# Performance work log

Measured on AMD Instinct MI355X. Metric: run time of the kernel, lower is better.

The kernel has to match this reference:

```python
import jax, jax.numpy as jnp
import numpy as np

B, CIN, H, W = 16, 20, 256, 256
WIDTH, M1, M2, NLAYERS, FC_HID, COUT = 64, 16, 16, 4, 128, 20


def setup_inputs() -> dict:
    key = jax.random.key(0)
    ks = jax.random.split(key, 16)
    scale = 1.0 / (WIDTH * WIDTH)  # matches torch: scale * rand(..., cfloat)
    u = lambda k, s: scale * jax.random.uniform(k, s, dtype=jnp.float32)
    n = lambda k, s: 0.05 * jax.random.normal(k, s, dtype=jnp.float32)
    return {
        "x": jax.random.normal(ks[0], (B, CIN, H, W), dtype=jnp.float32),
        # complex spectral weights stored as real/imag pairs, stacked over 4 layers
        "spec_w1r": u(ks[1], (NLAYERS, WIDTH, WIDTH, M1, M2)),
        "spec_w1i": u(ks[2], (NLAYERS, WIDTH, WIDTH, M1, M2)),
        "spec_w2r": u(ks[3], (NLAYERS, WIDTH, WIDTH, M1, M2)),
        "spec_w2i": u(ks[4], (NLAYERS, WIDTH, WIDTH, M1, M2)),
        # 1x1 conv weights (out, in) and biases, stacked over 4 layers
        "pw_w": n(ks[5], (NLAYERS, WIDTH, WIDTH)),
        "pw_b": n(ks[6], (NLAYERS, WIDTH)),
        "fc0_w": n(ks[7], (WIDTH, CIN)),
        "fc0_b": n(ks[8], (WIDTH,)),
        "fc1_w": n(ks[9], (FC_HID, WIDTH)),
        "fc1_b": n(ks[10], (FC_HID,)),
        "fc2_w": n(ks[11], (COUT, FC_HID)),
        "fc2_b": n(ks[12], (COUT,)),
    }


def _spectral_conv(h, w1, w2):
    # h: (B, WIDTH, H, W) real; w1,w2: (WIDTH, WIDTH, M1, M2) complex
    b, c, hh, ww = h.shape
    x_ft = jnp.fft.rfft2(h)  # (B, WIDTH, H, W//2+1) complex64
    top = jnp.einsum('bixy,ioxy->boxy', x_ft[:, :, :M1, :M2], w1)
    bot = jnp.einsum('bixy,ioxy->boxy', x_ft[:, :, -M1:, :M2], w2)
    out_ft = jnp.zeros((b, c, hh, ww // 2 + 1), dtype=jnp.complex64)
    out_ft = out_ft.at[:, :, :M1, :M2].set(top).at[:, :, -M1:, :M2].set(bot)
    return jnp.fft.irfft2(out_ft, s=(hh, ww))


def reference(x, spec_w1r, spec_w1i, spec_w2r, spec_w2i, pw_w, pw_b,
              fc0_w, fc0_b, fc1_w, fc1_b, fc2_w, fc2_b):
    gelu = lambda t: jax.nn.gelu(t, approximate=False)  # torch F.gelu default = erf
    # lift: permute to channels-last, Linear(20->width), back to channels-first
    h = jnp.einsum('bchw,dc->bdhw', x, fc0_w) + fc0_b[None, :, None, None]
    for i in range(NLAYERS):
        w1 = spec_w1r[i] + 1j * spec_w1i[i]
        w2 = spec_w2r[i] + 1j * spec_w2i[i]
        x1 = _spectral_conv(h, w1, w2)
        x2 = jnp.einsum('bihw,oi->bohw', h, pw_w[i]) + pw_b[i][None, :, None, None]
        h = x1 + x2
        if i < NLAYERS - 1:  # no GELU after the 4th block in the original
            h = gelu(h)
    h = jnp.einsum('bchw,dc->bdhw', h, fc1_w) + fc1_b[None, :, None, None]
    h = gelu(h)
    h = jnp.einsum('bchw,dc->bdhw', h, fc2_w) + fc2_b[None, :, None, None]
    return h  # (B, 20, H, W)
```

## Files before the change

kernel.cpp:

```cpp
#include <hip/hip_runtime.h>
#include <hip/hip_bf16.h>


#define HW_TOT 65536
#define PI2_256 0.024543692606170259758f

__device__ __forceinline__ float gelu_exact(float v) {
    return 0.5f * v * (1.0f + erff(v * 0.70710678118654752440f));
}
__device__ __forceinline__ float gelu_fast(float v) {
    float z  = v * 0.70710678118654752440f;
    float az = fabsf(z);
    float t  = __builtin_amdgcn_rcpf(fmaf(0.3275911f, az, 1.0f));
    float p  = t * (0.254829592f + t * (-0.284496736f + t * (1.421413741f +
               t * (-1.453152027f + t * 1.061405429f))));
    float e  = __expf(-az * az);
    float er = copysignf(1.0f - p * e, z);
    return 0.5f * v * (1.0f + er);
}
#define F4COMP(v, k) ((k)==0?(v).x:(k)==1?(v).y:(k)==2?(v).z:(v).w)

template<int CI, int CO, int WS>
__global__ void __launch_bounds__(256) conv1x1_kernel(
    const float* __restrict__ in, const float* __restrict__ w,
    const float* __restrict__ bias, float* __restrict__ out)
{
    const int b = blockIdx.y;
    const int p = blockIdx.x * 256 + threadIdx.x;
    const float* inp = in + (size_t)b * CI * HW_TOT + p;
    float acc[CO];
#pragma unroll
    for (int o = 0; o < CO; ++o) acc[o] = bias[o];
    for (int ci = 0; ci < CI; ++ci) {
        float hv = inp[(size_t)ci * HW_TOT];
#pragma unroll
        for (int o = 0; o < CO; ++o)
            acc[o] = fmaf(w[o * WS + ci], hv, acc[o]);
    }
    float* op = out + (size_t)b * CO * HW_TOT + p;
#pragma unroll
    for (int o = 0; o < CO; ++o) op[(size_t)o * HW_TOT] = acc[o];
}

__global__ void __launch_bounds__(256) dfty_kernel(
    const float* __restrict__ h, float* __restrict__ T)
{
    __shared__ float As[128][68];
    __shared__ float Wc[64][32];
    __shared__ float cs2[256], sn2[256];
    const int t = threadIdx.x;
    {
        float a = (float)t * PI2_256;
        cs2[t] = cosf(a); sn2[t] = sinf(a);
    }
    __syncthreads();

    const size_t rowbase = (size_t)blockIdx.x * 128;
    const int jg = t & 7, rg = t >> 3;
    float acc[4][4];
#pragma unroll
    for (int k = 0; k < 4; ++k)
#pragma unroll
        for (int q = 0; q < 4; ++q) acc[k][q] = 0.0f;

    for (int yc = 0; yc < 256; yc += 64) {
        if (yc) __syncthreads();
#pragma unroll
        for (int it = 0; it < 8; ++it) {
            int idx = t + 256 * it;
            int rr = idx >> 4, c4 = idx & 15;
            float4 v = *(const float4*)(h + (rowbase + rr) * 256 + yc + c4 * 4);
            *(float4*)&As[rr][c4 * 4] = v;
        }
#pragma unroll
        for (int it = 0; it < 8; ++it) {
            int i = t + 256 * it;
            int yl = i >> 5, j = i & 31, ky = j >> 1;
            int m = ((yc + yl) * ky) & 255;
            Wc[yl][j] = (j & 1) ? -sn2[m] : cs2[m];
        }
        __syncthreads();
#pragma unroll 2
        for (int yy = 0; yy < 64; yy += 4) {
            float4 wv[4], av[4];
#pragma unroll
            for (int q = 0; q < 4; ++q) wv[q] = *(const float4*)&Wc[yy + q][jg * 4];
#pragma unroll
            for (int k = 0; k < 4; ++k) av[k] = *(const float4*)&As[rg + 32 * k][yy];
#pragma unroll
            for (int k = 0; k < 4; ++k)
#pragma unroll
                for (int q = 0; q < 4; ++q) {
                    float a = F4COMP(av[k], q);
                    acc[k][0] = fmaf(a, wv[q].x, acc[k][0]);
                    acc[k][1] = fmaf(a, wv[q].y, acc[k][1]);
                    acc[k][2] = fmaf(a, wv[q].z, acc[k][2]);
                    acc[k][3] = fmaf(a, wv[q].w, acc[k][3]);
                }
        }
    }
#pragma unroll
    for (int k = 0; k < 4; ++k) {
        float4 v = make_float4(acc[k][0], acc[k][1], acc[k][2], acc[k][3]);
        *(float4*)&T[(rowbase + rg + 32 * k) * 32 + jg * 4] = v;
    }
}

__global__ void __launch_bounds__(512) dft2_kernel(
    const float2* __restrict__ T2, float2* __restrict__ X2)
{
    __shared__ float cs[256], sn[256];
    const int t = threadIdx.x;
    if (t < 256) {
        float a = (float)t * PI2_256;
        cs[t] = cosf(a); sn[t] = sinf(a);
    }
    __syncthreads();
    const int bc = blockIdx.x;
    const int ky = t & 15, kxi = t >> 4;
    const int kx = (kxi < 16) ? kxi : (224 + kxi);
    const float2* Tp = T2 + (size_t)bc * 4096 + ky;
    float xr = 0.0f, xi = 0.0f;
    int m = 0;
    for (int x = 0; x < 256; ++x) {
        float2 tv = Tp[(size_t)x * 16];
        float c = cs[m], s = sn[m];
        xr = fmaf(tv.x, c, fmaf(tv.y, s, xr));
        xi = fmaf(tv.y, c, fmaf(-tv.x, s, xi));
        m = (m + kx) & 255;
    }
    X2[(size_t)bc * 512 + t] = make_float2(xr, xi);
}

__global__ void __launch_bounds__(512) mix_kernel(
    const float2* __restrict__ X2, float2* __restrict__ Y2,
    const float* __restrict__ w1r, const float* __restrict__ w1i,
    const float* __restrict__ w2r, const float* __restrict__ w2i, int layer)
{
    const int bo = blockIdx.x;
    const int b = bo >> 6, o = bo & 63;
    const int t = threadIdx.x;
    const int ky = t & 15, kxi = t >> 4;
    const bool top = (kxi < 16);
    const int kxm = top ? kxi : (kxi - 16);
    const float* wr = top ? w1r : w2r;
    const float* wi = top ? w1i : w2i;
    float yr = 0.0f, yi = 0.0f;
    for (int i = 0; i < 64; ++i) {
        float2 xv = X2[((size_t)(b * 64 + i) * 32 + kxi) * 16 + ky];
        size_t widx = (((size_t)layer * 64 + i) * 64 + o) * 256 + (kxm * 16 + ky);
        float wrv = wr[widx], wiv = wi[widx];
        yr = fmaf(xv.x, wrv, fmaf(-xv.y, wiv, yr));
        yi = fmaf(xv.x, wiv, fmaf(xv.y, wrv, yi));
    }
    Y2[((size_t)(b * 64 + o) * 32 + kxi) * 16 + ky] = make_float2(yr, yi);
}

__global__ void __launch_bounds__(256) idft1_kernel(
    const float2* __restrict__ Y2, float2* __restrict__ G2)
{
    __shared__ float cs[256], sn[256];
    const int t = threadIdx.x;
    {
        float a = (float)t * PI2_256;
        cs[t] = cosf(a); sn[t] = sinf(a);
    }
    __syncthreads();
    const int bo = blockIdx.x >> 4;
    const int xc = blockIdx.x & 15;
    const int ky = t & 15, xo = t >> 4;
    const int x = xc * 16 + xo;
    const float2* Yp = Y2 + (size_t)bo * 512 + ky;
    float gr = 0.0f, gi = 0.0f;
    for (int kxi = 0; kxi < 32; ++kxi) {
        float2 yv = Yp[(size_t)kxi * 16];
        int kx = (kxi < 16) ? kxi : (224 + kxi);
        int m = (kx * x) & 255;
        float c = cs[m], s = sn[m];
        gr = fmaf(yv.x, c, fmaf(-yv.y, s, gr));
        gi = fmaf(yv.x, s, fmaf(yv.y, c, gi));
    }
    G2[((size_t)bo * 256 + x) * 16 + ky] = make_float2(gr, gi);
}

__global__ void __launch_bounds__(1024, 8) pwcomb_kernel(
    float* __restrict__ h, const float2* __restrict__ G2,
    const float* __restrict__ pw_w, const float* __restrict__ pw_b,
    int layer, int do_gelu)
{
    __shared__ float buf[20480];
    float (*hs)[256] = (float (*)[256])buf;
    float (*Wt)[64]  = (float (*)[64])(buf + 16384);
    float (*Gt)[64]  = (float (*)[64])buf;
    float (*Pt)[256] = (float (*)[256])(buf + 2048);
    const int t = threadIdx.x;
    const int b = blockIdx.x >> 8;
    const int x = blockIdx.x & 255;

    const float* wl = pw_w + layer * 4096;
#pragma unroll
    for (int it = 0; it < 4; ++it) {
        int i = t + 1024 * it;
        int o = i & 63, ci = i >> 6;
        Wt[ci][o] = wl[o * 64 + ci];
    }
#pragma unroll
    for (int it = 0; it < 4; ++it) {
        int idx = t + 1024 * it;
        int ci = idx >> 6, c4 = idx & 63;
        float4 v = *(const float4*)(h + ((size_t)(b * 64 + ci) * 256 + x) * 256 + c4 * 4);
        *(float4*)&hs[ci][c4 * 4] = v;
    }
    __syncthreads();

    const int og = t & 15, yg = t >> 4;
    const float* bl = pw_b + layer * 64;
    float acc[4][4];
#pragma unroll
    for (int oj = 0; oj < 4; ++oj) {
        float bv = bl[og * 4 + oj];
#pragma unroll
        for (int yj = 0; yj < 4; ++yj) acc[yj][oj] = bv;
    }
    for (int ci = 0; ci < 64; ++ci) {
        float4 hv = *(const float4*)&hs[ci][yg * 4];
        float4 wv = *(const float4*)&Wt[ci][og * 4];
#pragma unroll
        for (int yj = 0; yj < 4; ++yj) {
            float a = F4COMP(hv, yj);
            acc[yj][0] = fmaf(a, wv.x, acc[yj][0]);
            acc[yj][1] = fmaf(a, wv.y, acc[yj][1]);
            acc[yj][2] = fmaf(a, wv.z, acc[yj][2]);
            acc[yj][3] = fmaf(a, wv.w, acc[yj][3]);
        }
    }
    __syncthreads();

    {
        int o = t >> 4, ky = t & 15;
        float2 g = G2[((size_t)(b * 64 + o) * 256 + x) * 16 + ky];
        Gt[2 * ky][o] = g.x;
        Gt[2 * ky + 1][o] = g.y;
    }
    const float inv = 1.0f / 65536.0f;
#pragma unroll
    for (int it = 0; it < 8; ++it) {
        int i = t + 1024 * it;
        int jp = i >> 8, y = i & 255, ky = jp >> 1;
        int m = (ky * y) & 255;
        float wk = (ky == 0) ? inv : 2.0f * inv;
        float ang = (float)m * PI2_256;
        Pt[jp][y] = (jp & 1) ? -wk * sinf(ang) : wk * cosf(ang);
    }
    __syncthreads();

#pragma unroll 4
    for (int jp = 0; jp < 32; ++jp) {
        float4 pv = *(const float4*)&Pt[jp][yg * 4];
        float4 gv = *(const float4*)&Gt[jp][og * 4];
#pragma unroll
        for (int yj = 0; yj < 4; ++yj) {
            float a = F4COMP(pv, yj);
            acc[yj][0] = fmaf(a, gv.x, acc[yj][0]);
            acc[yj][1] = fmaf(a, gv.y, acc[yj][1]);
            acc[yj][2] = fmaf(a, gv.z, acc[yj][2]);
            acc[yj][3] = fmaf(a, gv.w, acc[yj][3]);
        }
    }
#pragma unroll
    for (int oj = 0; oj < 4; ++oj) {
        float4 v;
        v.x = acc[0][oj]; v.y = acc[1][oj]; v.z = acc[2][oj]; v.w = acc[3][oj];
        if (do_gelu) {
            v.x = gelu_fast(v.x); v.y = gelu_fast(v.y);
            v.z = gelu_fast(v.z); v.w = gelu_fast(v.w);
        }
        *(float4*)&h[((size_t)(b * 64 + og * 4 + oj) * 256 + x) * 256 + yg * 4] = v;
    }
}

__global__ void __launch_bounds__(256) transpose_w1_kernel(
    const float* __restrict__ w1, float* __restrict__ w1t)
{
    int i = blockIdx.x * 256 + threadIdx.x;
    int ci = i >> 7, hd = i & 127;
    w1t[i] = w1[hd * 64 + ci];
}

__global__ void __launch_bounds__(512, 4) proj_kernel(
    const float* __restrict__ h,
    const float* __restrict__ w1t, const float* __restrict__ b1,
    const float* __restrict__ w2, const float* __restrict__ b2,
    float* __restrict__ out)
{
    __shared__ float hs[64][128];
    __shared__ float red[4][20][128];
    const int t = threadIdx.x;
    const int blk = blockIdx.x;
    const int b = blk >> 9;
    const int p0 = (blk & 511) << 7;

    {
        const float* hp = h + (size_t)b * 64 * HW_TOT + p0;
#pragma unroll
        for (int it = 0; it < 4; ++it) {
            int idx = t + 512 * it;
            int ci = idx >> 5, c4 = idx & 31;
            float4 v = *(const float4*)(hp + (size_t)ci * HW_TOT + c4 * 4);
            *(float4*)&hs[ci][c4 * 4] = v;
        }
    }
    __syncthreads();

    const int px = t & 127;
    const int wv = __builtin_amdgcn_readfirstlane(t >> 7);
    const int hd0 = wv * 32;

    float acc[32];
#pragma unroll
    for (int k = 0; k < 32; ++k) acc[k] = b1[hd0 + k];
#pragma unroll 2
    for (int ci = 0; ci < 64; ++ci) {
        float a = hs[ci][px];
        const float* wr = w1t + ci * 128 + hd0;
#pragma unroll
        for (int k = 0; k < 32; ++k) acc[k] = fmaf(wr[k], a, acc[k]);
    }
#pragma unroll
    for (int k = 0; k < 32; ++k) acc[k] = gelu_fast(acc[k]);

    float acc2[20];
#pragma unroll
    for (int o = 0; o < 20; ++o) {
        const float* w2r = w2 + o * 128 + hd0;
        float s0 = (wv == 0) ? b2[o] : 0.0f, s1 = 0.0f;
#pragma unroll
        for (int k = 0; k < 32; k += 2) {
            s0 = fmaf(w2r[k], acc[k], s0);
            s1 = fmaf(w2r[k + 1], acc[k + 1], s1);
        }
        acc2[o] = s0 + s1;
    }
#pragma unroll
    for (int o = 0; o < 20; ++o) red[wv][o][px] = acc2[o];
    __syncthreads();

    const int og = t >> 7;
    float* op = out + (size_t)b * 20 * HW_TOT + p0 + px;
#pragma unroll
    for (int j = 0; j < 5; ++j) {
        int o = og * 5 + j;
        float s = red[0][o][px] + red[1][o][px] + red[2][o][px] + red[3][o][px];
        op[(size_t)o * HW_TOT] = s;
    }
}

extern "C" void kernel_launch(void* const* d_in, const int* in_sizes, int n_in,
                              void* d_out, int out_size, void* d_ws, size_t ws_size,
                              hipStream_t stream)
{
    const float* x     = (const float*)d_in[0];
    const float* w1r   = (const float*)d_in[1];
    const float* w1i   = (const float*)d_in[2];
    const float* w2r   = (const float*)d_in[3];
    const float* w2i   = (const float*)d_in[4];
    const float* pw_w  = (const float*)d_in[5];
    const float* pw_b  = (const float*)d_in[6];
    const float* fc0_w = (const float*)d_in[7];
    const float* fc0_b = (const float*)d_in[8];
    const float* fc1_w = (const float*)d_in[9];
    const float* fc1_b = (const float*)d_in[10];
    const float* fc2_w = (const float*)d_in[11];
    const float* fc2_b = (const float*)d_in[12];
    float* out = (float*)d_out;
    float* ws  = (float*)d_ws;

    const size_t per_sample_floats = 4849664;
    int CB = 16;
    while (CB > 1 && (size_t)CB * per_sample_floats * 4 > ws_size) CB >>= 1;

    float*  h  = ws;
    float*  T  = ws + (size_t)CB * 4194304;
    float2* T2 = (float2*)T;
    float2* X2 = (float2*)(T + (size_t)CB * 524288);
    float2* Y2 = (float2*)(T + (size_t)CB * 524288 + (size_t)CB * 65536);
    float2* G2 = T2;

    for (int c0 = 0; c0 < 16; c0 += CB) {
        const float* xc = x + (size_t)c0 * 20 * HW_TOT;
        float* oc = out + (size_t)c0 * 20 * HW_TOT;

        conv1x1_kernel<20, 64, 20>
            <<<dim3(256, CB), 256, 0, stream>>>(xc, fc0_w, fc0_b, h);

        for (int l = 0; l < 4; ++l) {
            dfty_kernel <<<CB * 128, 256, 0, stream>>>(h, T);
            dft2_kernel <<<CB * 64, 512, 0, stream>>>(T2, X2);
            mix_kernel  <<<CB * 64, 512, 0, stream>>>(X2, Y2, w1r, w1i, w2r, w2i, l);
            idft1_kernel<<<CB * 64 * 16, 256, 0, stream>>>(Y2, G2);
            pwcomb_kernel<<<CB * 256, 1024, 0, stream>>>(h, G2, pw_w, pw_b, l, (l < 3) ? 1 : 0);
        }

        transpose_w1_kernel<<<32, 256, 0, stream>>>(fc1_w, T);
        proj_kernel<<<CB * 512, 512, 0, stream>>>(h, T, fc1_b, fc2_w, fc2_b, oc);
    }
}
```

Baseline: 2.613 ms.

## Fuse final projection MLP into last layer's pointwise-combine kernel

The last FNO layer's pwcomb kernel now keeps its output tile in shared memory and directly applies the fc1+GELU+fc2 projection, writing the final output. This removes the write of h after layer 4 and the separate proj_kernel's reread of it, roughly 256MB of HBM traffic per chunk. The fused kernel runs at 1024 threads, which adds register pressure and extra syncs. The transposed fc1 weights go into the Y2 buffer, which is safe because idft1 has already consumed it.

```diff
diff --git a/kernel.cpp b/kernel.cpp
--- a/kernel.cpp
+++ b/kernel.cpp
@@ -183,10 +183,14 @@
     G2[((size_t)bo * 256 + x) * 16 + ky] = make_float2(gr, gi);
 }
 
+template<int FUSE>
 __global__ void __launch_bounds__(1024, 8) pwcomb_kernel(
     float* __restrict__ h, const float2* __restrict__ G2,
     const float* __restrict__ pw_w, const float* __restrict__ pw_b,
-    int layer, int do_gelu)
+    int layer, int do_gelu,
+    const float* __restrict__ w1t, const float* __restrict__ fb1,
+    const float* __restrict__ fw2, const float* __restrict__ fb2,
+    float* __restrict__ out)
 {
     __shared__ float buf[20480];
     float (*hs)[256] = (float (*)[256])buf;
@@ -267,15 +271,74 @@
             acc[yj][3] = fmaf(a, gv.w, acc[yj][3]);
         }
     }
+
+    if (!FUSE) {
+#pragma unroll
+        for (int oj = 0; oj < 4; ++oj) {
+            float4 v;
+            v.x = acc[0][oj]; v.y = acc[1][oj]; v.z = acc[2][oj]; v.w = acc[3][oj];
+            if (do_gelu) {
+                v.x = gelu_fast(v.x); v.y = gelu_fast(v.y);
+                v.z = gelu_fast(v.z); v.w = gelu_fast(v.w);
+            }
+            *(float4*)&h[((size_t)(b * 64 + og * 4 + oj) * 256 + x) * 256 + yg * 4] = v;
+        }
+        return;
+    }
+
+    __syncthreads();
 #pragma unroll
     for (int oj = 0; oj < 4; ++oj) {
-        float4 v;
-        v.x = acc[0][oj]; v.y = acc[1][oj]; v.z = acc[2][oj]; v.w = acc[3][oj];
-        if (do_gelu) {
-            v.x = gelu_fast(v.x); v.y = gelu_fast(v.y);
-            v.z = gelu_fast(v.z); v.w = gelu_fast(v.w);
-        }
-        *(float4*)&h[((size_t)(b * 64 + og * 4 + oj) * 256 + x) * 256 + yg * 4] = v;
+        float4 v = make_float4(acc[0][oj], acc[1][oj], acc[2][oj], acc[3][oj]);
+        *(float4*)&buf[(og * 4 + oj) * 260 + yg * 4] = v;
+    }
+    __syncthreads();
+
+    const int px = t & 255;
+    const int wf = __builtin_amdgcn_readfirstlane(t >> 8);
+    float acc2[20];
+#pragma unroll
+    for (int o = 0; o < 20; ++o) acc2[o] = (wf == 0) ? fb2[o] : 0.0f;
+
+#pragma unroll
+    for (int pass = 0; pass < 2; ++pass) {
+        const int hd0 = wf * 32 + pass * 16;
+        float fa[16];
+#pragma unroll
+        for (int k = 0; k < 16; ++k) fa[k] = fb1[hd0 + k];
+#pragma unroll 2
+        for (int ci = 0; ci < 64; ++ci) {
+            float a = buf[ci * 260 + px];
+            const float* wr = w1t + ci * 128 + hd0;
+#pragma unroll
+            for (int k = 0; k < 16; ++k) fa[k] = fmaf(wr[k], a, fa[k]);
+        }
+#pragma unroll
+        for (int k = 0; k < 16; ++k) fa[k] = gelu_fast(fa[k]);
+#pragma unroll
+        for (int o = 0; o < 20; ++o) {
+            const float* w2r = fw2 + o * 128 + hd0;
+            float s0 = 0.0f, s1 = 0.0f;
+#pragma unroll
+            for (int k = 0; k < 16; k += 2) {
+                s0 = fmaf(w2r[k], fa[k], s0);
+                s1 = fmaf(w2r[k + 1], fa[k + 1], s1);
+            }
+            acc2[o] += s0 + s1;
+        }
+    }
+    __syncthreads();
+#pragma unroll
+    for (int o = 0; o < 20; ++o) buf[(wf * 20 + o) * 256 + px] = acc2[o];
+    __syncthreads();
+
+    float* op = out + (size_t)b * 20 * HW_TOT + x * 256 + px;
+#pragma unroll
+    for (int j = 0; j < 5; ++j) {
+        int o = wf * 5 + j;
+        float s = buf[o * 256 + px] + buf[(20 + o) * 256 + px]
+                + buf[(40 + o) * 256 + px] + buf[(60 + o) * 256 + px];
+        op[(size_t)o * HW_TOT] = s;
     }
 }
 
@@ -285,74 +348,6 @@
     int i = blockIdx.x * 256 + threadIdx.x;
     int ci = i >> 7, hd = i & 127;
     w1t[i] = w1[hd * 64 + ci];
-}
-
-__global__ void __launch_bounds__(512, 4) proj_kernel(
-    const float* __restrict__ h,
-    const float* __restrict__ w1t, const float* __restrict__ b1,
-    const float* __restrict__ w2, const float* __restrict__ b2,
-    float* __restrict__ out)
-{
-    __shared__ float hs[64][128];
-    __shared__ float red[4][20][128];
-    const int t = threadIdx.x;
-    const int blk = blockIdx.x;
-    const int b = blk >> 9;
-    const int p0 = (blk & 511) << 7;
-
-    {
-        const float* hp = h + (size_t)b * 64 * HW_TOT + p0;
-#pragma unroll
-        for (int it = 0; it < 4; ++it) {
-            int idx = t + 512 * it;
-            int ci = idx >> 5, c4 = idx & 31;
-            float4 v = *(const float4*)(hp + (size_t)ci * HW_TOT + c4 * 4);
-            *(float4*)&hs[ci][c4 * 4] = v;
-        }
-    }
-    __syncthreads();
-
-    const int px = t & 127;
-    const int wv = __builtin_amdgcn_readfirstlane(t >> 7);
-    const int hd0 = wv * 32;
-
-    float acc[32];
-#pragma unroll
-    for (int k = 0; k < 32; ++k) acc[k] = b1[hd0 + k];
-#pragma unroll 2
-    for (int ci = 0; ci < 64; ++ci) {
-        float a = hs[ci][px];
-        const float* wr = w1t + ci * 128 + hd0;
-#pragma unroll
-        for (int k = 0; k < 32; ++k) acc[k] = fmaf(wr[k], a, acc[k]);
-    }
-#pragma unroll
-    for (int k = 0; k < 32; ++k) acc[k] = gelu_fast(acc[k]);
-
-    float acc2[20];
-#pragma unroll
-    for (int o = 0; o < 20; ++o) {
-        const float* w2r = w2 + o * 128 + hd0;
-        float s0 = (wv == 0) ? b2[o] : 0.0f, s1 = 0.0f;
-#pragma unroll
-        for (int k = 0; k < 32; k += 2) {
-            s0 = fmaf(w2r[k], acc[k], s0);
-            s1 = fmaf(w2r[k + 1], acc[k + 1], s1);
-        }
-        acc2[o] = s0 + s1;
-    }
-#pragma unroll
-    for (int o = 0; o < 20; ++o) red[wv][o][px] = acc2[o];
-    __syncthreads();
-
-    const int og = t >> 7;
-    float* op = out + (size_t)b * 20 * HW_TOT + p0 + px;
-#pragma unroll
-    for (int j = 0; j < 5; ++j) {
-        int o = og * 5 + j;
-        float s = red[0][o][px] + red[1][o][px] + red[2][o][px] + red[3][o][px];
-        op[(size_t)o * HW_TOT] = s;
-    }
 }
 
 extern "C" void kernel_launch(void* const* d_in, const int* in_sizes, int n_in,
@@ -393,15 +388,24 @@
         conv1x1_kernel<20, 64, 20>
             <<<dim3(256, CB), 256, 0, stream>>>(xc, fc0_w, fc0_b, h);
 
-        for (int l = 0; l < 4; ++l) {
+        for (int l = 0; l < 3; ++l) {
             dfty_kernel <<<CB * 128, 256, 0, stream>>>(h, T);
             dft2_kernel <<<CB * 64, 512, 0, stream>>>(T2, X2);
             mix_kernel  <<<CB * 64, 512, 0, stream>>>(X2, Y2, w1r, w1i, w2r, w2i, l);
             idft1_kernel<<<CB * 64 * 16, 256, 0, stream>>>(Y2, G2);
-            pwcomb_kernel<<<CB * 256, 1024, 0, stream>>>(h, G2, pw_w, pw_b, l, (l < 3) ? 1 : 0);
-        }
-
-        transpose_w1_kernel<<<32, 256, 0, stream>>>(fc1_w, T);
-        proj_kernel<<<CB * 512, 512, 0, stream>>>(h, T, fc1_b, fc2_w, fc2_b, oc);
-    }
-}
+            pwcomb_kernel<0><<<CB * 256, 1024, 0, stream>>>(
+                h, G2, pw_w, pw_b, l, 1,
+                nullptr, nullptr, nullptr, nullptr, nullptr);
+        }
+
+        dfty_kernel <<<CB * 128, 256, 0, stream>>>(h, T);
+        dft2_kernel <<<CB * 64, 512, 0, stream>>>(T2, X2);
+        mix_kernel  <<<CB * 64, 512, 0, stream>>>(X2, Y2, w1r, w1i, w2r, w2i, 3);
+        idft1_kernel<<<CB * 64 * 16, 256, 0, stream>>>(Y2, G2);
+        float* w1t_buf = (float*)Y2;
+        transpose_w1_kernel<<<32, 256, 0, stream>>>(fc1_w, w1t_buf);
+        pwcomb_kernel<1><<<CB * 256, 1024, 0, stream>>>(
+            h, G2, pw_w, pw_b, 3, 0,
+            w1t_buf, fc1_b, fc2_w, fc2_b, oc);
+    }
+}
```

After: 2.457 ms. 1.06x faster.
